# Optimization experiments

Measured on AMD Instinct MI355X. Metric: run time of the kernel, lower is better.

The kernel has to match this reference:

```python
import jax, jax.numpy as jnp
import numpy as np

DIM = 1024
HEADS = 16
HEAD_DIM = DIM // HEADS
HIDDEN = int(DIM * 4.0)
EPS = 1e-5


def layernorm(x, w, b):
    m = jnp.mean(x, axis=-1, keepdims=True)
    v = jnp.var(x, axis=-1, keepdims=True)
    return (x - m) * jax.lax.rsqrt(v + EPS) * w + b


def apply_rope(t, pos):
    # t: [B, H, S, D], pos: [B, S] int
    half = t.shape[-1] // 2
    inv_freq = 1.0 / (10000.0 ** (jnp.arange(half, dtype=jnp.float32) / half))
    ang = pos.astype(jnp.float32)[:, None, :, None] * inv_freq  # [B,1,S,half]
    cos = jnp.cos(ang)
    sin = jnp.sin(ang)
    t1, t2 = t[..., :half], t[..., half:]
    return jnp.concatenate([t1 * cos - t2 * sin, t2 * cos + t1 * sin], axis=-1)


def setup_inputs() -> dict:
    key = jax.random.key(0)
    ks = jax.random.split(key, 10)
    B, S = 2, 2048
    x = jax.random.normal(ks[0], (B, S, DIM), dtype=jnp.float32)
    pos = jnp.sort(jax.random.randint(ks[1], (B, S), 0, 2048), axis=-1).astype(jnp.int32)
    def lin(k, fi, fo):
        return jax.random.normal(k, (fi, fo), dtype=jnp.float32) / np.sqrt(fi)
    return {
        "x": x,
        "pos": pos,
        "ln1_w": jnp.ones((DIM,), jnp.float32),
        "ln1_b": jnp.zeros((DIM,), jnp.float32),
        "qkv_w": lin(ks[2], DIM, 3 * DIM),
        "qkv_b": jnp.zeros((3 * DIM,), jnp.float32),
        "o_w": lin(ks[3], DIM, DIM),
        "o_b": jnp.zeros((DIM,), jnp.float32),
        "ln2_w": jnp.ones((DIM,), jnp.float32),
        "ln2_b": jnp.zeros((DIM,), jnp.float32),
        "mlp_w1": lin(ks[4], DIM, HIDDEN),
        "mlp_b1": jnp.zeros((HIDDEN,), jnp.float32),
        "mlp_w2": lin(ks[5], HIDDEN, DIM),
        "mlp_b2": jnp.zeros((DIM,), jnp.float32),
    }


def reference(x, pos, ln1_w, ln1_b, qkv_w, qkv_b, o_w, o_b, ln2_w, ln2_b, mlp_w1, mlp_b1, mlp_w2, mlp_b2):
    B, S, C = x.shape
    scale = HEAD_DIM ** -0.5
    xn = layernorm(x, ln1_w, ln1_b)
    qkv = (xn @ qkv_w + qkv_b).reshape(B, S, 3, HEADS, HEAD_DIM)
    qkv = jnp.transpose(qkv, (2, 0, 3, 1, 4))  # [3,B,H,S,D]
    q, k, v = qkv[0], qkv[1], qkv[2]
    q = apply_rope(q, pos)
    k = apply_rope(k, pos)
    scores = jnp.einsum("bhsd,bhtd->bhst", q, k) * scale
    probs = jax.nn.softmax(scores, axis=-1)
    attn = jnp.einsum("bhst,bhtd->bhsd", probs, v)
    attn = jnp.transpose(attn, (0, 2, 1, 3)).reshape(B, S, C)
    x = x + attn @ o_w + o_b
    xn2 = layernorm(x, ln2_w, ln2_b)
    h = jax.nn.gelu(xn2 @ mlp_w1 + mlp_b1, approximate=False)
    x = x + h @ mlp_w2 + mlp_b2
    return x
```

## Files before the change

### kernel.cpp

```cpp
#include <hip/hip_runtime.h>
#include <hip/hip_bf16.h>
#include <math.h>

#define DIMC 1024
#define HEADS 16
#define HD 64
#define HIDDEN 4096
#define BATCH 2
#define SEQ 2048
#define TOK (BATCH*SEQ)

typedef unsigned short u16;
typedef __attribute__((ext_vector_type(8))) short short8;
typedef __attribute__((ext_vector_type(4))) float f32x4;

__device__ __forceinline__ u16 f2bf(float f) {
  unsigned u = __float_as_uint(f);
  u += 0x7fff + ((u >> 16) & 1);
  return (u16)(u >> 16);
}
__device__ __forceinline__ float bf2f(u16 h) {
  return __uint_as_float(((unsigned)h) << 16);
}

__device__ __forceinline__ void gl_lds16(const void* g, void* l) {
  __builtin_amdgcn_global_load_lds(
      (__attribute__((address_space(1))) void*)g,
      (__attribute__((address_space(3))) void*)l, 16, 0, 0);
}

__device__ __forceinline__ const short8* lds_row128(const u16* base, int row, int chunk) {
  return (const short8*)((const char*)base + row * 128 + (((chunk) ^ (row & 7)) << 4));
}

__global__ __launch_bounds__(256) void ln_kernel(
    const float* __restrict__ x, const float* __restrict__ w,
    const float* __restrict__ b, u16* __restrict__ out)
{
  int row = blockIdx.x, tid = threadIdx.x;
  const float4* xr = (const float4*)(x + (size_t)row * DIMC);
  float4 v = xr[tid];
  float s = v.x + v.y + v.z + v.w;
  float s2 = v.x*v.x + v.y*v.y + v.z*v.z + v.w*v.w;
  for (int off = 32; off > 0; off >>= 1) {
    s  += __shfl_down(s, off);
    s2 += __shfl_down(s2, off);
  }
  __shared__ float red[8];
  int lane = tid & 63, wv = tid >> 6;
  if (lane == 0) { red[wv] = s; red[4 + wv] = s2; }
  __syncthreads();
  float S  = red[0] + red[1] + red[2] + red[3];
  float S2 = red[4] + red[5] + red[6] + red[7];
  float mean = S * (1.f / DIMC);
  float var  = S2 * (1.f / DIMC) - mean * mean;
  float inv  = rsqrtf(var + 1e-5f);
  int base = tid * 4;
  float vv[4] = {v.x, v.y, v.z, v.w};
#pragma unroll
  for (int j = 0; j < 4; ++j)
    out[(size_t)row * DIMC + base + j] = f2bf((vv[j] - mean) * inv * w[base + j] + b[base + j]);
}

__global__ __launch_bounds__(256) void transpose_cast(
    const float* __restrict__ W, u16* __restrict__ Wt, int K, int N)
{
  __shared__ float t[32][33];
  int n0 = blockIdx.x * 32, k0 = blockIdx.y * 32;
  for (int r = threadIdx.y; r < 32; r += 8)
    t[r][threadIdx.x] = W[(size_t)(k0 + r) * N + n0 + threadIdx.x];
  __syncthreads();
  for (int r = threadIdx.y; r < 32; r += 8)
    Wt[(size_t)(n0 + r) * K + k0 + threadIdx.x] = f2bf(t[threadIdx.x][r]);
}

template<int EPI>
__global__ __launch_bounds__(256) void gemm_bt(
    const u16* __restrict__ A, const u16* __restrict__ Bt,
    const float* __restrict__ bias, const float* __restrict__ res,
    u16* __restrict__ outb, float* __restrict__ outf,
    int M, int N, int K)
{
  __shared__ u16 shm[16384];
  u16* As[2] = { shm,        shm + 4096 };
  u16* Bs[2] = { shm + 8192, shm + 12288 };
  int tid = threadIdx.x;
  int lane = tid & 63, w = tid >> 6;
  int m0 = blockIdx.y * 128, n0 = blockIdx.x * 128;
  int wr = w >> 1, wc = w & 1;
  f32x4 acc[4][4] = {};

  int trow = tid >> 2;
  int tk = (((tid & 3) ^ ((tid >> 3) & 3)) * 8);
  const u16* ga = A  + (size_t)(m0 + trow) * K + tk;
  const u16* gb = Bt + (size_t)(n0 + trow) * K + tk;
  int rofs = lane & 15, q4 = lane >> 4;
  int ach = ((q4 ^ ((rofs >> 1) & 3)) << 4);
  int nt = K >> 5;

#define G_STAGE(BUF) do { \
    gl_lds16(ga, As[BUF] + tid * 8); \
    gl_lds16(ga + (size_t)64 * K, As[BUF] + tid * 8 + 2048); \
    gl_lds16(gb, Bs[BUF] + tid * 8); \
    gl_lds16(gb + (size_t)64 * K, Bs[BUF] + tid * 8 + 2048); \
    ga += 32; gb += 32; } while (0)

#define G_COMPUTE(BUF) do { \
    short8 af[4], bfr[4]; \
    _Pragma("unroll") for (int mm = 0; mm < 4; ++mm) \
      af[mm] = *(const short8*)((const char*)As[BUF] + (wr * 64 + mm * 16 + rofs) * 64 + ach); \
    _Pragma("unroll") for (int nn = 0; nn < 4; ++nn) \
      bfr[nn] = *(const short8*)((const char*)Bs[BUF] + (wc * 64 + nn * 16 + rofs) * 64 + ach); \
    _Pragma("unroll") for (int mm = 0; mm < 4; ++mm) \
      _Pragma("unroll") for (int nn = 0; nn < 4; ++nn) \
        acc[mm][nn] = __builtin_amdgcn_mfma_f32_16x16x32_bf16(af[mm], bfr[nn], acc[mm][nn], 0, 0, 0); \
    } while (0)

  G_STAGE(0);
  __syncthreads();
  for (int t = 0; t < nt; t += 2) {
    if (t + 1 < nt) G_STAGE(1);
    G_COMPUTE(0);
    __syncthreads();
    if (t + 2 < nt) G_STAGE(0);
    G_COMPUTE(1);
    __syncthreads();
  }
#undef G_STAGE
#undef G_COMPUTE

  if (EPI == 0 || EPI == 1) {
    u16* C = shm;
#pragma unroll
    for (int nn = 0; nn < 4; ++nn) {
      int ccol = wc * 64 + nn * 16 + rofs;
      float bv = bias[n0 + ccol];
#pragma unroll
      for (int mm = 0; mm < 4; ++mm)
#pragma unroll
        for (int r = 0; r < 4; ++r) {
          int crow = wr * 64 + mm * 16 + q4 * 4 + r;
          float v = acc[mm][nn][r] + bv;
          if (EPI == 1) v = 0.5f * v * (1.f + erff(v * 0.70710678118f));
          C[crow * 128 + ccol] = f2bf(v);
        }
    }
    __syncthreads();
    for (int c = tid; c < 2048; c += 256) {
      int row = c >> 4, off = (c & 15) * 8;
      *(short8*)(outb + (size_t)(m0 + row) * N + n0 + off) = *(const short8*)&C[row * 128 + off];
    }
  } else {
    float* Cf = (float*)shm;
#pragma unroll
    for (int p = 0; p < 2; ++p) {
      if (wr == p) {
#pragma unroll
        for (int nn = 0; nn < 4; ++nn) {
          int ccol = wc * 64 + nn * 16 + rofs;
          float bv = bias[n0 + ccol];
#pragma unroll
          for (int mm = 0; mm < 4; ++mm)
#pragma unroll
            for (int r = 0; r < 4; ++r)
              Cf[(mm * 16 + q4 * 4 + r) * 128 + ccol] = acc[mm][nn][r] + bv;
        }
      }
      __syncthreads();
      for (int c = tid; c < 2048; c += 256) {
        int row = c >> 5, off = (c & 31) * 4;
        size_t idx = (size_t)(m0 + p * 64 + row) * N + n0 + off;
        float4 rv = *(const float4*)(res + idx);
        float4 cv = *(const float4*)&Cf[row * 128 + off];
        cv.x += rv.x; cv.y += rv.y; cv.z += rv.z; cv.w += rv.w;
        *(float4*)(outf + idx) = cv;
      }
      __syncthreads();
    }
  }
}

__global__ __launch_bounds__(256) void rope_split(
    const u16* __restrict__ qkv, const int* __restrict__ pos,
    u16* __restrict__ Q, u16* __restrict__ Kk, u16* __restrict__ Vt)
{
  int st = blockIdx.x, bh = blockIdx.y;
  int b = bh >> 4, hh = bh & 15;
  int s0 = st * 64;
  int tid = threadIdx.x;
  __shared__ u16 vtile[64][72];

  for (int i = tid; i < 64 * 32; i += 256) {
    int sl = i >> 5, dp = i & 31;
    int s = s0 + sl;
    float p = (float)pos[b * SEQ + s];
    float freq = exp2f((float)dp * -0.4152410118609203f);
    float ang = p * freq;
    float sn, c;
    __sincosf(ang, &sn, &c);
    const u16* qr = qkv + (size_t)(b * SEQ + s) * 3072 + hh * 64;
    float q1 = bf2f(qr[dp]),        q2 = bf2f(qr[dp + 32]);
    float k1 = bf2f(qr[1024 + dp]), k2 = bf2f(qr[1024 + dp + 32]);
    size_t ob = ((size_t)bh * SEQ + s) * HD;
    const float QS = 0.18033688011112042f;
    Q[ob + dp]       = f2bf((q1 * c - q2 * sn) * QS);
    Q[ob + dp + 32]  = f2bf((q2 * c + q1 * sn) * QS);
    Kk[ob + dp]      = f2bf(k1 * c - k2 * sn);
    Kk[ob + dp + 32] = f2bf(k2 * c + k1 * sn);
  }
  for (int i = tid; i < 64 * 64; i += 256) {
    int sl = i >> 6, d = i & 63;
    vtile[d][sl] = qkv[(size_t)(b * SEQ + s0 + sl) * 3072 + 2048 + hh * 64 + d];
  }
  __syncthreads();
  for (int i = tid; i < 64 * 64; i += 256) {
    int d = i >> 6, sl = i & 63;
    Vt[((size_t)bh * HD + d) * SEQ + s0 + sl] = vtile[d][sl];
  }
}

__global__ __launch_bounds__(256) void attn_kernel(
    const u16* __restrict__ Q, const u16* __restrict__ K,
    const u16* __restrict__ Vt, u16* __restrict__ O)
{
  __shared__ u16 Ks[2][64 * 64];
  __shared__ u16 Vs[2][64 * 64];
  __shared__ u16 Ps[4 * 16 * 64];
  int qt = blockIdx.x, bh = blockIdx.y;
  int b = bh >> 4, hh = bh & 15;
  const u16* Qp = Q + ((size_t)bh * SEQ + qt * 64) * HD;
  const u16* Kp = K + (size_t)bh * SEQ * HD;
  const u16* Vp = Vt + (size_t)bh * HD * SEQ;
  int tid = threadIdx.x, lane = tid & 63, w = tid >> 6;
  int rofs = lane & 15, q4 = lane >> 4;
  int kofs = q4 * 8;

  short8 aq0 = *(const short8*)&Qp[(w * 16 + rofs) * HD + kofs];
  short8 aq1 = *(const short8*)&Qp[(w * 16 + rofs) * HD + 32 + kofs];

  short8 ones;
#pragma unroll
  for (int j = 0; j < 8; ++j) ones[j] = (short)0x3F80;

  f32x4 o[4] = {};
  f32x4 lsum = {};

  int srow = tid >> 3;
  int sg0 = ((tid & 7) ^ (srow & 7)) * 8;
  u16* pw = &Ps[w * 16 * 64];

#define A_STAGE(BUF, T0) do { \
    gl_lds16(Kp + (size_t)((T0) + srow) * HD + sg0, &Ks[BUF][tid * 8]); \
    gl_lds16(Kp + (size_t)((T0) + 32 + srow) * HD + sg0, &Ks[BUF][tid * 8 + 2048]); \
    gl_lds16(Vp + (size_t)srow * SEQ + (T0) + sg0, &Vs[BUF][tid * 8]); \
    gl_lds16(Vp + (size_t)(32 + srow) * SEQ + (T0) + sg0, &Vs[BUF][tid * 8 + 2048]); \
  } while (0)

  auto tile = [&](const u16* KsB, const u16* VsB) {
    f32x4 s[4] = {};
#pragma unroll
    for (int n = 0; n < 4; ++n) {
      int krow = n * 16 + rofs;
      short8 bk0 = *lds_row128(KsB, krow, q4);
      short8 bk1 = *lds_row128(KsB, krow, 4 + q4);
      s[n] = __builtin_amdgcn_mfma_f32_16x16x32_bf16(aq0, bk0, s[n], 0, 0, 0);
      s[n] = __builtin_amdgcn_mfma_f32_16x16x32_bf16(aq1, bk1, s[n], 0, 0, 0);
    }
#pragma unroll
    for (int n = 0; n < 4; ++n)
#pragma unroll
      for (int r = 0; r < 4; ++r) {
        int prow = q4 * 4 + r;
        int pbyte = (n * 16 + rofs) * 2;
        float p = __builtin_amdgcn_exp2f(s[n][r]);
        *(u16*)((char*)pw + prow * 128 + (pbyte ^ ((prow & 7) << 4))) = f2bf(p);
      }
    short8 pa0 = *lds_row128(pw, rofs, q4);
    short8 pa1 = *lds_row128(pw, rofs, 4 + q4);
    lsum = __builtin_amdgcn_mfma_f32_16x16x32_bf16(pa0, ones, lsum, 0, 0, 0);
    lsum = __builtin_amdgcn_mfma_f32_16x16x32_bf16(pa1, ones, lsum, 0, 0, 0);
#pragma unroll
    for (int n = 0; n < 4; ++n) {
      int vrow = n * 16 + rofs;
      short8 bv0 = *lds_row128(VsB, vrow, q4);
      short8 bv1 = *lds_row128(VsB, vrow, 4 + q4);
      o[n] = __builtin_amdgcn_mfma_f32_16x16x32_bf16(pa0, bv0, o[n], 0, 0, 0);
      o[n] = __builtin_amdgcn_mfma_f32_16x16x32_bf16(pa1, bv1, o[n], 0, 0, 0);
    }
  };

  A_STAGE(0, 0);
  __syncthreads();
  for (int t0 = 0; t0 < SEQ; t0 += 128) {
    if (t0 + 64 < SEQ) A_STAGE(1, t0 + 64);
    tile(Ks[0], Vs[0]);
    __syncthreads();
    if (t0 + 128 < SEQ) A_STAGE(0, t0 + 128);
    tile(Ks[1], Vs[1]);
    __syncthreads();
  }
#undef A_STAGE

#pragma unroll
  for (int r = 0; r < 4; ++r) {
    float inv = 1.f / lsum[r];
    int lrow = w * 16 + q4 * 4 + r;
#pragma unroll
    for (int n = 0; n < 4; ++n)
      Ps[lrow * 64 + n * 16 + rofs] = f2bf(o[n][r] * inv);
  }
  __syncthreads();
  for (int c = tid; c < 512; c += 256) {
    int row = c >> 3, off = (c & 7) * 8;
    int sq = qt * 64 + row;
    *(short8*)(O + ((size_t)b * SEQ + sq) * DIMC + hh * 64 + off) = *(const short8*)&Ps[row * 64 + off];
  }
}

extern "C" void kernel_launch(void* const* d_in, const int* in_sizes, int n_in,
                              void* d_out, int out_size, void* d_ws, size_t ws_size,
                              hipStream_t stream) {
  const float* x     = (const float*)d_in[0];
  const int*   pos   = (const int*)  d_in[1];
  const float* ln1_w = (const float*)d_in[2];
  const float* ln1_b = (const float*)d_in[3];
  const float* qkv_w = (const float*)d_in[4];
  const float* qkv_b = (const float*)d_in[5];
  const float* o_w   = (const float*)d_in[6];
  const float* o_b   = (const float*)d_in[7];
  const float* ln2_w = (const float*)d_in[8];
  const float* ln2_b = (const float*)d_in[9];
  const float* w1    = (const float*)d_in[10];
  const float* b1    = (const float*)d_in[11];
  const float* w2    = (const float*)d_in[12];
  const float* b2    = (const float*)d_in[13];
  float* out = (float*)d_out;

  char* ws = (char*)d_ws;
  u16* WqkvT = (u16*)(ws + 0);
  u16* WoT   = (u16*)(ws + 6291456);
  u16* W1T   = (u16*)(ws + 8388608);
  u16* W2T   = (u16*)(ws + 16777216);
  u16* xn    = (u16*)(ws + 25165824);
  u16* qkvbf = (u16*)(ws + 33554432);
  u16* Qb    = (u16*)(ws + 58720256);
  u16* Kb    = (u16*)(ws + 67108864);
  u16* Vtb   = (u16*)(ws + 75497472);
  u16* attnb = (u16*)(ws + 83886080);
  u16* hbuf  = (u16*)(ws + 25165824);
  float* x2  = (float*)(ws + 58720256);
  u16* xn2   = (u16*)(ws + 75497472);

  transpose_cast<<<dim3(3072/32, 1024/32), dim3(32, 8), 0, stream>>>(qkv_w, WqkvT, 1024, 3072);
  transpose_cast<<<dim3(1024/32, 1024/32), dim3(32, 8), 0, stream>>>(o_w,  WoT,  1024, 1024);
  transpose_cast<<<dim3(4096/32, 1024/32), dim3(32, 8), 0, stream>>>(w1,   W1T,  1024, 4096);
  transpose_cast<<<dim3(1024/32, 4096/32), dim3(32, 8), 0, stream>>>(w2,   W2T,  4096, 1024);

  ln_kernel<<<TOK, 256, 0, stream>>>(x, ln1_w, ln1_b, xn);
  gemm_bt<0><<<dim3(24, 32), 256, 0, stream>>>(xn, WqkvT, qkv_b, nullptr, qkvbf, nullptr, 4096, 3072, 1024);
  rope_split<<<dim3(32, 32), 256, 0, stream>>>(qkvbf, pos, Qb, Kb, Vtb);
  attn_kernel<<<dim3(32, 32), 256, 0, stream>>>(Qb, Kb, Vtb, attnb);
  gemm_bt<2><<<dim3(8, 32), 256, 0, stream>>>(attnb, WoT, o_b, x, nullptr, x2, 4096, 1024, 1024);
  ln_kernel<<<TOK, 256, 0, stream>>>(x2, ln2_w, ln2_b, xn2);
  gemm_bt<1><<<dim3(32, 32), 256, 0, stream>>>(xn2, W1T, b1, nullptr, hbuf, nullptr, 4096, 4096, 1024);
  gemm_bt<2><<<dim3(8, 32), 256, 0, stream>>>(hbuf, W2T, b2, x2, nullptr, out, 4096, 1024, 4096);
}
```

Measured before the change: 290.6 us.

## Add 256x256-tile direct-to-LDS GEMM for QKV and MLP-up projections

Adds a new 512-thread GEMM kernel with 256x256 output tiles, XOR-swizzled LDS layout, global-to-LDS async loads with vmcnt-based double buffering, and s_setprio around MFMA bursts. It replaces the 128x128 kernel for the QKV and first MLP GEMMs, and the old kernel is reduced to the residual-fp32 epilogue path only. Larger tiles raise arithmetic intensity and cut LDS traffic per FLOP. In exchange the grid is much smaller (192 and 256 blocks), which can leave CUs underutilized, and register pressure from a 32-accumulator-per-thread tile may be high.

```diff
diff --git a/kernel.cpp b/kernel.cpp
--- a/kernel.cpp
+++ b/kernel.cpp
@@ -72,6 +72,107 @@
   __syncthreads();
   for (int r = threadIdx.y; r < 32; r += 8)
     Wt[(size_t)(n0 + r) * K + k0 + threadIdx.x] = f2bf(t[threadIdx.x][r]);
+}
+
+template<int EPI>
+__global__ __launch_bounds__(512, 2) void gemm256(
+    const u16* __restrict__ A, const u16* __restrict__ Bt,
+    const float* __restrict__ bias, u16* __restrict__ outb,
+    int M, int N, int K)
+{
+  __shared__ u16 AB[2][2][256 * 64];
+  int tid = threadIdx.x;
+  int lane = tid & 63, wid = tid >> 6;
+  int wr = wid >> 2, wn = wid & 3;
+  int rofs = lane & 15, q4 = lane >> 4;
+  int m0 = blockIdx.y * 256, n0 = blockIdx.x * 256;
+  int mb = wr * 128, nb = wn * 64;
+
+  f32x4 acc[8][4] = {};
+
+  int off[4];
+#pragma unroll
+  for (int j = 0; j < 4; ++j) {
+    int p = tid + j * 512;
+    int row = p >> 3;
+    int cl = (p & 7) ^ (row & 7);
+    off[j] = row * K + cl * 8;
+  }
+  const u16* gA = A  + (size_t)m0 * K;
+  const u16* gB = Bt + (size_t)n0 * K;
+
+#define G_STAGE(B_, T_) do { \
+    _Pragma("unroll") for (int j = 0; j < 4; ++j) { \
+      int p8 = (tid + j * 512) * 8; \
+      gl_lds16(gA + off[j] + (T_) * 64, &AB[B_][0][p8]); \
+      gl_lds16(gB + off[j] + (T_) * 64, &AB[B_][1][p8]); \
+    } } while (0)
+
+#define G_COMP(B_) do { \
+    const char* Ab = (const char*)&AB[B_][0][0]; \
+    const char* Bb = (const char*)&AB[B_][1][0]; \
+    _Pragma("unroll") for (int mg = 0; mg < 2; ++mg) { \
+      short8 a[4][2]; \
+      _Pragma("unroll") for (int mm = 0; mm < 4; ++mm) \
+        _Pragma("unroll") for (int kk = 0; kk < 2; ++kk) { \
+          int row = mb + (mg * 4 + mm) * 16 + rofs; \
+          a[mm][kk] = *(const short8*)(Ab + row * 128 + ((((kk << 2) | q4) ^ (row & 7)) << 4)); \
+        } \
+      _Pragma("unroll") for (int np = 0; np < 2; ++np) { \
+        short8 bb[2][2]; \
+        _Pragma("unroll") for (int nn = 0; nn < 2; ++nn) \
+          _Pragma("unroll") for (int kk = 0; kk < 2; ++kk) { \
+            int row = nb + (np * 2 + nn) * 16 + rofs; \
+            bb[nn][kk] = *(const short8*)(Bb + row * 128 + ((((kk << 2) | q4) ^ (row & 7)) << 4)); \
+          } \
+        __builtin_amdgcn_s_setprio(1); \
+        _Pragma("unroll") for (int mm = 0; mm < 4; ++mm) \
+          _Pragma("unroll") for (int nn = 0; nn < 2; ++nn) \
+            _Pragma("unroll") for (int kk = 0; kk < 2; ++kk) \
+              acc[mg * 4 + mm][np * 2 + nn] = __builtin_amdgcn_mfma_f32_16x16x32_bf16( \
+                  a[mm][kk], bb[nn][kk], acc[mg * 4 + mm][np * 2 + nn], 0, 0, 0); \
+        __builtin_amdgcn_s_setprio(0); \
+      } \
+    } } while (0)
+
+  G_STAGE(0, 0);
+  G_STAGE(1, 1);
+  int NT = K >> 6;
+  for (int t = 0; t < NT; ++t) {
+    int b = t & 1;
+    if (t + 1 < NT) asm volatile("s_waitcnt vmcnt(8)" ::: "memory");
+    else            asm volatile("s_waitcnt vmcnt(0)" ::: "memory");
+    __builtin_amdgcn_s_barrier();
+    asm volatile("" ::: "memory");
+    G_COMP(b);
+    asm volatile("" ::: "memory");
+    __builtin_amdgcn_s_barrier();
+    asm volatile("" ::: "memory");
+    if (t + 2 < NT) G_STAGE(b, t + 2);
+  }
+#undef G_STAGE
+#undef G_COMP
+
+  u16* Ct = &AB[0][0][0];
+#pragma unroll
+  for (int nn = 0; nn < 4; ++nn) {
+    int ccol = nb + nn * 16 + rofs;
+    float bv = bias[n0 + ccol];
+#pragma unroll
+    for (int m = 0; m < 8; ++m)
+#pragma unroll
+      for (int r = 0; r < 4; ++r) {
+        int row = mb + m * 16 + q4 * 4 + r;
+        float v = acc[m][nn][r] + bv;
+        if (EPI == 1) v = 0.5f * v * (1.f + erff(v * 0.70710678118f));
+        Ct[row * 256 + ccol] = f2bf(v);
+      }
+  }
+  __syncthreads();
+  for (int c = tid; c < 256 * 32; c += 512) {
+    int row = c >> 5, offb = (c & 31) * 8;
+    *(short8*)(outb + (size_t)(m0 + row) * N + n0 + offb) = *(const short8*)&Ct[row * 256 + offb];
+  }
 }
 
 template<int EPI>
@@ -129,54 +230,31 @@
 #undef G_STAGE
 #undef G_COMPUTE
 
-  if (EPI == 0 || EPI == 1) {
-    u16* C = shm;
-#pragma unroll
-    for (int nn = 0; nn < 4; ++nn) {
-      int ccol = wc * 64 + nn * 16 + rofs;
-      float bv = bias[n0 + ccol];
-#pragma unroll
-      for (int mm = 0; mm < 4; ++mm)
-#pragma unroll
-        for (int r = 0; r < 4; ++r) {
-          int crow = wr * 64 + mm * 16 + q4 * 4 + r;
-          float v = acc[mm][nn][r] + bv;
-          if (EPI == 1) v = 0.5f * v * (1.f + erff(v * 0.70710678118f));
-          C[crow * 128 + ccol] = f2bf(v);
-        }
+  float* Cf = (float*)shm;
+#pragma unroll
+  for (int p = 0; p < 2; ++p) {
+    if (wr == p) {
+#pragma unroll
+      for (int nn = 0; nn < 4; ++nn) {
+        int ccol = wc * 64 + nn * 16 + rofs;
+        float bv = bias[n0 + ccol];
+#pragma unroll
+        for (int mm = 0; mm < 4; ++mm)
+#pragma unroll
+          for (int r = 0; r < 4; ++r)
+            Cf[(mm * 16 + q4 * 4 + r) * 128 + ccol] = acc[mm][nn][r] + bv;
+      }
     }
     __syncthreads();
     for (int c = tid; c < 2048; c += 256) {
-      int row = c >> 4, off = (c & 15) * 8;
-      *(short8*)(outb + (size_t)(m0 + row) * N + n0 + off) = *(const short8*)&C[row * 128 + off];
+      int row = c >> 5, off = (c & 31) * 4;
+      size_t idx = (size_t)(m0 + p * 64 + row) * N + n0 + off;
+      float4 rv = *(const float4*)(res + idx);
+      float4 cv = *(const float4*)&Cf[row * 128 + off];
+      cv.x += rv.x; cv.y += rv.y; cv.z += rv.z; cv.w += rv.w;
+      *(float4*)(outf + idx) = cv;
     }
-  } else {
-    float* Cf = (float*)shm;
-#pragma unroll
-    for (int p = 0; p < 2; ++p) {
-      if (wr == p) {
-#pragma unroll
-        for (int nn = 0; nn < 4; ++nn) {
-          int ccol = wc * 64 + nn * 16 + rofs;
-          float bv = bias[n0 + ccol];
-#pragma unroll
-          for (int mm = 0; mm < 4; ++mm)
-#pragma unroll
-            for (int r = 0; r < 4; ++r)
-              Cf[(mm * 16 + q4 * 4 + r) * 128 + ccol] = acc[mm][nn][r] + bv;
-        }
-      }
-      __syncthreads();
-      for (int c = tid; c < 2048; c += 256) {
-        int row = c >> 5, off = (c & 31) * 4;
-        size_t idx = (size_t)(m0 + p * 64 + row) * N + n0 + off;
-        float4 rv = *(const float4*)(res + idx);
-        float4 cv = *(const float4*)&Cf[row * 128 + off];
-        cv.x += rv.x; cv.y += rv.y; cv.z += rv.z; cv.w += rv.w;
-        *(float4*)(outf + idx) = cv;
-      }
-      __syncthreads();
-    }
+    __syncthreads();
   }
 }
 
@@ -357,11 +435,11 @@
   transpose_cast<<<dim3(1024/32, 4096/32), dim3(32, 8), 0, stream>>>(w2,   W2T,  4096, 1024);
 
   ln_kernel<<<TOK, 256, 0, stream>>>(x, ln1_w, ln1_b, xn);
-  gemm_bt<0><<<dim3(24, 32), 256, 0, stream>>>(xn, WqkvT, qkv_b, nullptr, qkvbf, nullptr, 4096, 3072, 1024);
+  gemm256<0><<<dim3(12, 16), 512, 0, stream>>>(xn, WqkvT, qkv_b, qkvbf, 4096, 3072, 1024);
   rope_split<<<dim3(32, 32), 256, 0, stream>>>(qkvbf, pos, Qb, Kb, Vtb);
   attn_kernel<<<dim3(32, 32), 256, 0, stream>>>(Qb, Kb, Vtb, attnb);
   gemm_bt<2><<<dim3(8, 32), 256, 0, stream>>>(attnb, WoT, o_b, x, nullptr, x2, 4096, 1024, 1024);
   ln_kernel<<<TOK, 256, 0, stream>>>(x2, ln2_w, ln2_b, xn2);
-  gemm_bt<1><<<dim3(32, 32), 256, 0, stream>>>(xn2, W1T, b1, nullptr, hbuf, nullptr, 4096, 4096, 1024);
+  gemm256<1><<<dim3(16, 16), 512, 0, stream>>>(xn2, W1T, b1, hbuf, 4096, 4096, 1024);
   gemm_bt<2><<<dim3(8, 32), 256, 0, stream>>>(hbuf, W2T, b2, x2, nullptr, out, 4096, 1024, 4096);
 }
```

Result: slower. 313.2 us (+7.8%).

## Add BM=64 GEMM tile for N=1024 GEMMs and swizzle workgroup order

Applied to the files above, without the earlier changes.

Templates the GEMM on the M tile height and uses 64-row tiles for the output-projection and MLP-down GEMMs, doubling their workgroup count so more CUs stay busy. It also remaps workgroup IDs into XCD-aware 4x4 tile groups to improve L2 locality of A/B tiles. Smaller tiles lower per-block arithmetic intensity and increase redundant B loads.

```diff
diff --git a/kernel.cpp b/kernel.cpp
--- a/kernel.cpp
+++ b/kernel.cpp
@@ -74,21 +74,32 @@
     Wt[(size_t)(n0 + r) * K + k0 + threadIdx.x] = f2bf(t[threadIdx.x][r]);
 }
 
-template<int EPI>
+template<int EPI, int BM>
 __global__ __launch_bounds__(256) void gemm_bt(
     const u16* __restrict__ A, const u16* __restrict__ Bt,
     const float* __restrict__ bias, const float* __restrict__ res,
     u16* __restrict__ outb, float* __restrict__ outf,
     int M, int N, int K)
 {
-  __shared__ u16 shm[16384];
-  u16* As[2] = { shm,        shm + 4096 };
-  u16* Bs[2] = { shm + 8192, shm + 12288 };
+  constexpr int AMM = BM / 32;
+  constexpr int HALF = BM / 2;
+  __shared__ u16 shm[(BM + 128) * 32 * 2];
+  u16* As[2] = { shm,             shm + BM * 32 };
+  u16* Bs[2] = { shm + 2 * BM * 32, shm + 2 * BM * 32 + 128 * 32 };
   int tid = threadIdx.x;
   int lane = tid & 63, w = tid >> 6;
-  int m0 = blockIdx.y * 128, n0 = blockIdx.x * 128;
   int wr = w >> 1, wc = w & 1;
-  f32x4 acc[4][4] = {};
+
+  int nwg = gridDim.x * gridDim.y;
+  int orig = blockIdx.y * gridDim.x + blockIdx.x;
+  int wg = (orig & 7) * (nwg >> 3) + (orig >> 3);
+  int gi = wg >> 4, wi = wg & 15;
+  int gx4 = gridDim.x >> 2;
+  int bx = (gi % gx4) * 4 + (wi & 3);
+  int by = (gi / gx4) * 4 + (wi >> 2);
+  int m0 = by * BM, n0 = bx * 128;
+
+  f32x4 acc[AMM][4] = {};
 
   int trow = tid >> 2;
   int tk = (((tid & 3) ^ ((tid >> 3) & 3)) * 8);
@@ -98,36 +109,38 @@
   int ach = ((q4 ^ ((rofs >> 1) & 3)) << 4);
   int nt = K >> 5;
 
-#define G_STAGE(BUF) do { \
-    gl_lds16(ga, As[BUF] + tid * 8); \
-    gl_lds16(ga + (size_t)64 * K, As[BUF] + tid * 8 + 2048); \
-    gl_lds16(gb, Bs[BUF] + tid * 8); \
-    gl_lds16(gb + (size_t)64 * K, Bs[BUF] + tid * 8 + 2048); \
-    ga += 32; gb += 32; } while (0)
-
-#define G_COMPUTE(BUF) do { \
-    short8 af[4], bfr[4]; \
-    _Pragma("unroll") for (int mm = 0; mm < 4; ++mm) \
-      af[mm] = *(const short8*)((const char*)As[BUF] + (wr * 64 + mm * 16 + rofs) * 64 + ach); \
-    _Pragma("unroll") for (int nn = 0; nn < 4; ++nn) \
-      bfr[nn] = *(const short8*)((const char*)Bs[BUF] + (wc * 64 + nn * 16 + rofs) * 64 + ach); \
-    _Pragma("unroll") for (int mm = 0; mm < 4; ++mm) \
-      _Pragma("unroll") for (int nn = 0; nn < 4; ++nn) \
-        acc[mm][nn] = __builtin_amdgcn_mfma_f32_16x16x32_bf16(af[mm], bfr[nn], acc[mm][nn], 0, 0, 0); \
-    } while (0)
-
-  G_STAGE(0);
+  auto stage = [&](int buf) {
+    gl_lds16(ga, As[buf] + tid * 8);
+    if (BM == 128) gl_lds16(ga + (size_t)64 * K, As[buf] + tid * 8 + 2048);
+    gl_lds16(gb, Bs[buf] + tid * 8);
+    gl_lds16(gb + (size_t)64 * K, Bs[buf] + tid * 8 + 2048);
+    ga += 32; gb += 32;
+  };
+  auto compute = [&](int buf) {
+    short8 af[AMM], bfr[4];
+#pragma unroll
+    for (int mm = 0; mm < AMM; ++mm)
+      af[mm] = *(const short8*)((const char*)As[buf] + (wr * HALF + mm * 16 + rofs) * 64 + ach);
+#pragma unroll
+    for (int nn = 0; nn < 4; ++nn)
+      bfr[nn] = *(const short8*)((const char*)Bs[buf] + (wc * 64 + nn * 16 + rofs) * 64 + ach);
+#pragma unroll
+    for (int mm = 0; mm < AMM; ++mm)
+#pragma unroll
+      for (int nn = 0; nn < 4; ++nn)
+        acc[mm][nn] = __builtin_amdgcn_mfma_f32_16x16x32_bf16(af[mm], bfr[nn], acc[mm][nn], 0, 0, 0);
+  };
+
+  stage(0);
   __syncthreads();
   for (int t = 0; t < nt; t += 2) {
-    if (t + 1 < nt) G_STAGE(1);
-    G_COMPUTE(0);
-    __syncthreads();
-    if (t + 2 < nt) G_STAGE(0);
-    G_COMPUTE(1);
-    __syncthreads();
-  }
-#undef G_STAGE
-#undef G_COMPUTE
+    if (t + 1 < nt) stage(1);
+    compute(0);
+    __syncthreads();
+    if (t + 2 < nt) stage(0);
+    compute(1);
+    __syncthreads();
+  }
 
   if (EPI == 0 || EPI == 1) {
     u16* C = shm;
@@ -136,17 +149,17 @@
       int ccol = wc * 64 + nn * 16 + rofs;
       float bv = bias[n0 + ccol];
 #pragma unroll
-      for (int mm = 0; mm < 4; ++mm)
+      for (int mm = 0; mm < AMM; ++mm)
 #pragma unroll
         for (int r = 0; r < 4; ++r) {
-          int crow = wr * 64 + mm * 16 + q4 * 4 + r;
+          int crow = wr * HALF + mm * 16 + q4 * 4 + r;
           float v = acc[mm][nn][r] + bv;
           if (EPI == 1) v = 0.5f * v * (1.f + erff(v * 0.70710678118f));
           C[crow * 128 + ccol] = f2bf(v);
         }
     }
     __syncthreads();
-    for (int c = tid; c < 2048; c += 256) {
+    for (int c = tid; c < BM * 16; c += 256) {
       int row = c >> 4, off = (c & 15) * 8;
       *(short8*)(outb + (size_t)(m0 + row) * N + n0 + off) = *(const short8*)&C[row * 128 + off];
     }
@@ -160,16 +173,16 @@
           int ccol = wc * 64 + nn * 16 + rofs;
           float bv = bias[n0 + ccol];
 #pragma unroll
-          for (int mm = 0; mm < 4; ++mm)
+          for (int mm = 0; mm < AMM; ++mm)
 #pragma unroll
             for (int r = 0; r < 4; ++r)
               Cf[(mm * 16 + q4 * 4 + r) * 128 + ccol] = acc[mm][nn][r] + bv;
         }
       }
       __syncthreads();
-      for (int c = tid; c < 2048; c += 256) {
+      for (int c = tid; c < HALF * 32; c += 256) {
         int row = c >> 5, off = (c & 31) * 4;
-        size_t idx = (size_t)(m0 + p * 64 + row) * N + n0 + off;
+        size_t idx = (size_t)(m0 + p * HALF + row) * N + n0 + off;
         float4 rv = *(const float4*)(res + idx);
         float4 cv = *(const float4*)&Cf[row * 128 + off];
         cv.x += rv.x; cv.y += rv.y; cv.z += rv.z; cv.w += rv.w;
@@ -357,11 +370,11 @@
   transpose_cast<<<dim3(1024/32, 4096/32), dim3(32, 8), 0, stream>>>(w2,   W2T,  4096, 1024);
 
   ln_kernel<<<TOK, 256, 0, stream>>>(x, ln1_w, ln1_b, xn);
-  gemm_bt<0><<<dim3(24, 32), 256, 0, stream>>>(xn, WqkvT, qkv_b, nullptr, qkvbf, nullptr, 4096, 3072, 1024);
+  gemm_bt<0,128><<<dim3(24, 32), 256, 0, stream>>>(xn, WqkvT, qkv_b, nullptr, qkvbf, nullptr, 4096, 3072, 1024);
   rope_split<<<dim3(32, 32), 256, 0, stream>>>(qkvbf, pos, Qb, Kb, Vtb);
   attn_kernel<<<dim3(32, 32), 256, 0, stream>>>(Qb, Kb, Vtb, attnb);
-  gemm_bt<2><<<dim3(8, 32), 256, 0, stream>>>(attnb, WoT, o_b, x, nullptr, x2, 4096, 1024, 1024);
+  gemm_bt<2,64><<<dim3(8, 64), 256, 0, stream>>>(attnb, WoT, o_b, x, nullptr, x2, 4096, 1024, 1024);
   ln_kernel<<<TOK, 256, 0, stream>>>(x2, ln2_w, ln2_b, xn2);
-  gemm_bt<1><<<dim3(32, 32), 256, 0, stream>>>(xn2, W1T, b1, nullptr, hbuf, nullptr, 4096, 4096, 1024);
-  gemm_bt<2><<<dim3(8, 32), 256, 0, stream>>>(hbuf, W2T, b2, x2, nullptr, out, 4096, 1024, 4096);
-}
+  gemm_bt<1,128><<<dim3(32, 32), 256, 0, stream>>>(xn2, W1T, b1, nullptr, hbuf, nullptr, 4096, 4096, 1024);
+  gemm_bt<2,64><<<dim3(8, 64), 256, 0, stream>>>(hbuf, W2T, b2, x2, nullptr, out, 4096, 1024, 4096);
+}
```

New measurement: 268.3 us. -7.7%, faster.
